# Kernel optimization log

Hardware: AMD Instinct MI355X
Metric: run time of the kernel (lower is better)

Reference implementation:

```python
import jax, jax.numpy as jnp
import numpy as np

EPS = 1e-5

def conv1x1(x, w):
    # x: [N,C,H,W], w: [O,C] (1x1 conv, no bias)
    return jnp.einsum('nchw,oc->nohw', x, w)

def bn_relu(x, gamma, beta, mean, var):
    # inference-mode BatchNorm2d + ReLU; params broadcast over H,W
    scale = gamma * jax.lax.rsqrt(var + EPS)
    y = (x - mean[:, None, None]) * scale[:, None, None] + beta[:, None, None]
    return jax.nn.relu(y)

def setup_inputs() -> dict:
    key = jax.random.key(0)
    ks = jax.random.split(key, 8)
    N, C, D, H, W = 4, 256, 9, 64, 64
    IC = C // 2
    return {
        'feature': jax.random.normal(ks[0], (N, C, D, H, W), dtype=jnp.float32),
        'w_theta': jax.random.normal(ks[1], (IC, C), dtype=jnp.float32) * 0.05,
        'bn_theta_gamma': jnp.ones((IC,), jnp.float32),
        'bn_theta_beta': jnp.zeros((IC,), jnp.float32),
        'bn_theta_mean': jax.random.normal(ks[2], (IC,), dtype=jnp.float32) * 0.1,
        'bn_theta_var': jax.random.uniform(ks[3], (IC,), dtype=jnp.float32, minval=0.5, maxval=1.5),
        'w_phi': jax.random.normal(ks[4], (IC, C), dtype=jnp.float32) * 0.05,
        'bn_phi_gamma': jnp.ones((IC,), jnp.float32),
        'bn_phi_beta': jnp.zeros((IC,), jnp.float32),
        'bn_phi_mean': jax.random.normal(ks[5], (IC,), dtype=jnp.float32) * 0.1,
        'bn_phi_var': jax.random.uniform(ks[6], (IC,), dtype=jnp.float32, minval=0.5, maxval=1.5),
        'w_g': jax.random.normal(ks[7], (IC, C), dtype=jnp.float32) * 0.05,
        'w_w': jax.random.normal(jax.random.fold_in(key, 99), (C, IC), dtype=jnp.float32) * 0.05,
    }

def reference(feature, w_theta, bn_theta_gamma, bn_theta_beta, bn_theta_mean, bn_theta_var,
              w_phi, bn_phi_gamma, bn_phi_beta, bn_phi_mean, bn_phi_var, w_g, w_w):
    N, C, D, H, W = feature.shape
    IC = w_theta.shape[0]
    center_x = feature[:, :, D // 2 + 1]               # [N,C,H,W]
    x = jnp.max(feature, axis=2)                       # max_pool3d (D,1,1) -> [N,C,H,W]

    theta = bn_relu(conv1x1(center_x, w_theta), bn_theta_gamma, bn_theta_beta, bn_theta_mean, bn_theta_var)
    phi = bn_relu(conv1x1(x, w_phi), bn_phi_gamma, bn_phi_beta, bn_phi_mean, bn_phi_var)
    g = conv1x1(x, w_g)

    HW = H * W
    theta_f = theta.reshape(N, IC, HW)                 # [N,IC,HW]
    phi_f = phi.reshape(N, IC, HW)
    g_f = g.reshape(N, IC, HW)

    f = jnp.einsum('ncq,nck->nqk', theta_f, phi_f)     # [N,HW,HW] unscaled scores
    weight = jax.nn.softmax(f, axis=-1)
    weighted = jnp.einsum('nqk,nck->ncq', weight, g_f) # [N,IC,HW]
    weighted = weighted.reshape(N, IC, H, W)

    out = conv1x1(weighted, w_w) + center_x            # residual
    return out
```

## Files before the change

### kernel.cpp

```cpp
#include <hip/hip_runtime.h>
#include <math.h>

#define HW   4096
#define CIN  256
#define ICH  128
#define NB   4
#define KSPL 6
#define KVB  32

typedef __attribute__((ext_vector_type(4))) float f32x4;
typedef __attribute__((ext_vector_type(8))) short bf16x8;
typedef __attribute__((ext_vector_type(4))) short bf16x4;
typedef __attribute__((ext_vector_type(4))) unsigned u32x4;

__device__ inline short f2bf(float f) {
    unsigned int u = __float_as_uint(f);
    u += 0x7fffU + ((u >> 16) & 1U);
    return (short)(u >> 16);
}

__device__ inline float bf2f(short s) {
    return __uint_as_float(((unsigned int)(unsigned short)s) << 16);
}

__device__ inline float exp2a(float x) {
    float r;
    asm("v_exp_f32 %0, %1" : "=v"(r) : "v"(x));
    return r;
}
__device__ inline float log2a(float x) {
    float r;
    asm("v_log_f32 %0, %1" : "=v"(r) : "v"(x));
    return r;
}
__device__ inline unsigned cvtpk(float a, float b) {
    unsigned r;
    asm("v_cvt_pk_bf16_f32 %0, %1, %2" : "=v"(r) : "v"(a), "v"(b));
    return r;
}

__device__ inline f32x4 mfma16(bf16x8 a, bf16x8 b, f32x4 c) {
    return __builtin_amdgcn_mfma_f32_16x16x32_bf16(a, b, c, 0, 0, 0);
}

__device__ inline bf16x8 ldf(const short* p) { return *(const bf16x8*)p; }

__global__ void k_prep_w(const float* __restrict__ wth, const float* __restrict__ wph,
                         const float* __restrict__ wg,  const float* __restrict__ ww,
                         const float* __restrict__ gth, const float* __restrict__ bth,
                         const float* __restrict__ mth, const float* __restrict__ vth,
                         const float* __restrict__ gph, const float* __restrict__ bph,
                         const float* __restrict__ mph, const float* __restrict__ vph,
                         short* __restrict__ wthb, short* __restrict__ wphb,
                         short* __restrict__ wgb,  short* __restrict__ wwb,
                         float* __restrict__ bnp) {
    const float LOG2E = 1.44269504f;
    int i = blockIdx.x * 256 + threadIdx.x;
    wthb[i] = f2bf(wth[i]);
    wphb[i] = f2bf(wph[i]);
    wgb[i]  = f2bf(wg[i]);
    wwb[i]  = f2bf(ww[i]);
    if (blockIdx.x == 0 && threadIdx.x < ICH) {
        int o = threadIdx.x;
        float s1 = gth[o] * rsqrtf(vth[o] + 1e-5f);
        bnp[o]        = s1 * LOG2E;
        bnp[ICH + o]  = (bth[o] - mth[o] * s1) * LOG2E;
        float s2 = gph[o] * rsqrtf(vph[o] + 1e-5f);
        bnp[2*ICH + o] = s2;
        bnp[3*ICH + o] = bph[o] - mph[o] * s2;
    }
}

__global__ __launch_bounds__(256) void k_prep_x(const float* __restrict__ feat,
                                                short* __restrict__ Xbf,
                                                short* __restrict__ CXbf) {
    const int q0 = blockIdx.x * 64;
    const int c0 = blockIdx.y * 32;
    const int n  = blockIdx.z;
    __shared__ float xs[32][68];
    __shared__ float cxs[32][68];
    const int tid = threadIdx.x;
    const int qv  = (tid & 15) * 4;
    const int ci  = tid >> 4;

    #pragma unroll
    for (int h = 0; h < 2; ++h) {
        const int cc = h * 16 + ci;
        const float* fp = feat + ((size_t)(n * CIN + c0 + cc)) * 9 * HW + q0 + qv;
        float4 mx = *(const float4*)fp;
        float4 cx = make_float4(0.f, 0.f, 0.f, 0.f);
        #pragma unroll
        for (int d = 1; d < 9; ++d) {
            float4 v = *(const float4*)(fp + (size_t)d * HW);
            if (d == 5) cx = v;
            mx.x = fmaxf(mx.x, v.x); mx.y = fmaxf(mx.y, v.y);
            mx.z = fmaxf(mx.z, v.z); mx.w = fmaxf(mx.w, v.w);
        }
        *(float4*)&xs[cc][qv]  = mx;
        *(float4*)&cxs[cc][qv] = cx;
    }
    __syncthreads();
    #pragma unroll
    for (int it = 0; it < 2; ++it) {
        const int q  = it * 32 + (tid >> 3);
        const int cq = (tid & 7) * 4;
        ushort4 ox, oc;
        ox.x = (unsigned short)f2bf(xs[cq][q]);
        ox.y = (unsigned short)f2bf(xs[cq + 1][q]);
        ox.z = (unsigned short)f2bf(xs[cq + 2][q]);
        ox.w = (unsigned short)f2bf(xs[cq + 3][q]);
        oc.x = (unsigned short)f2bf(cxs[cq][q]);
        oc.y = (unsigned short)f2bf(cxs[cq + 1][q]);
        oc.z = (unsigned short)f2bf(cxs[cq + 2][q]);
        oc.w = (unsigned short)f2bf(cxs[cq + 3][q]);
        const size_t ob = ((size_t)n * HW + q0 + q) * CIN + c0 + cq;
        *(ushort4*)&Xbf[ob]  = ox;
        *(ushort4*)&CXbf[ob] = oc;
    }
}

__global__ __launch_bounds__(256) void k_conv3(const short* __restrict__ Xbf,
                                               const short* __restrict__ CXbf,
                                               const short* __restrict__ wthb,
                                               const short* __restrict__ wphb,
                                               const short* __restrict__ wgb,
                                               const float* __restrict__ bnp,
                                               short* __restrict__ theta,
                                               short* __restrict__ phi,
                                               short* __restrict__ Vt) {
    const int n    = blockIdx.y;
    const int op   = blockIdx.z;
    const int wave = threadIdx.x >> 6;
    const int lane = threadIdx.x & 63;
    const int lr = lane & 15, lg = lane >> 4;
    const int q0 = blockIdx.x * 64 + wave * 16;
    const short* Xn  = Xbf  + (size_t)n * HW * CIN;
    const short* CXn = CXbf + (size_t)n * HW * CIN;

    f32x4 acc[8];
    #pragma unroll
    for (int i = 0; i < 8; ++i) { acc[i][0]=0.f; acc[i][1]=0.f; acc[i][2]=0.f; acc[i][3]=0.f; }

    if (op == 0) {
        short* thn = theta + (size_t)n * HW * ICH;
        #pragma unroll
        for (int cf = 0; cf < 8; ++cf) {
            bf16x8 a = ldf(CXn + (q0 + lr) * CIN + cf * 32 + lg * 8);
            #pragma unroll
            for (int of = 0; of < 8; ++of) {
                bf16x8 b = ldf(wthb + (of * 16 + lr) * CIN + cf * 32 + lg * 8);
                acc[of] = mfma16(a, b, acc[of]);
            }
        }
        #pragma unroll
        for (int of = 0; of < 8; ++of) {
            int o = of * 16 + lr;
            float sA = bnp[o], sB = bnp[ICH + o];
            #pragma unroll
            for (int r = 0; r < 4; ++r) {
                int q = q0 + lg * 4 + r;
                thn[q * ICH + o] = f2bf(fmaxf(acc[of][r] * sA + sB, 0.f));
            }
        }
    } else if (op == 1) {
        short* phn = phi + (size_t)n * HW * ICH;
        #pragma unroll
        for (int cf = 0; cf < 8; ++cf) {
            bf16x8 a = ldf(Xn + (q0 + lr) * CIN + cf * 32 + lg * 8);
            #pragma unroll
            for (int of = 0; of < 8; ++of) {
                bf16x8 b = ldf(wphb + (of * 16 + lr) * CIN + cf * 32 + lg * 8);
                acc[of] = mfma16(a, b, acc[of]);
            }
        }
        #pragma unroll
        for (int of = 0; of < 8; ++of) {
            int o = of * 16 + lr;
            float sA = bnp[2*ICH + o], sB = bnp[3*ICH + o];
            #pragma unroll
            for (int r = 0; r < 4; ++r) {
                int q = q0 + lg * 4 + r;
                phn[q * ICH + o] = f2bf(fmaxf(acc[of][r] * sA + sB, 0.f));
            }
        }
    } else {
        short* vtn = Vt + (size_t)n * ICH * HW;
        #pragma unroll
        for (int cf = 0; cf < 8; ++cf) {
            bf16x8 bx = ldf(Xn + (q0 + lr) * CIN + cf * 32 + lg * 8);
            #pragma unroll
            for (int mf = 0; mf < 8; ++mf) {
                bf16x8 a = ldf(wgb + (mf * 16 + lr) * CIN + cf * 32 + lg * 8);
                acc[mf] = mfma16(a, bx, acc[mf]);
            }
        }
        #pragma unroll
        for (int mf = 0; mf < 8; ++mf) {
            #pragma unroll
            for (int r = 0; r < 4; ++r) {
                int o = mf * 16 + lg * 4 + r;
                vtn[(size_t)o * HW + q0 + lr] = f2bf(acc[mf][r]);
            }
        }
    }
}

__global__ __launch_bounds__(256, 3) void k_attn(const short* __restrict__ theta,
                                                 const short* __restrict__ phi,
                                                 const short* __restrict__ Vt,
                                                 short* __restrict__ Op,
                                                 float* __restrict__ Ls) {
    __shared__ char  K_lds[2][8192];
    __shared__ short V_lds[2][128 * 40];

    const int bid  = blockIdx.x;
    const int j    = bid & 7;
    const int n    = j >> 1;
    const int rest = ((bid >> 3) << 1) | (j & 1);
    const int qb   = rest / KSPL;
    const int ks   = rest % KSPL;
    const int tbase = ks * 21 + (ks < 2 ? ks : 2);
    const int tcnt  = 21 + (ks < 2 ? 1 : 0);
    const int tid  = threadIdx.x;
    const int wave = tid >> 6;
    const int lane = tid & 63;
    const int lr = lane & 15, lg = lane >> 4;
    const int q0 = qb * 128 + wave * 32;

    const short* Qn = theta + (size_t)n * HW * ICH;
    const short* Kn = phi   + (size_t)n * HW * ICH;
    const short* Vn = Vt    + (size_t)n * ICH * HW;

    bf16x8 aq[2][4];
    #pragma unroll
    for (int m2 = 0; m2 < 2; ++m2)
        #pragma unroll
        for (int cf = 0; cf < 4; ++cf)
            aq[m2][cf] = ldf(Qn + (q0 + m2 * 16 + lr) * ICH + cf * 32 + lg * 8);

    f32x4 O[2][8];
    #pragma unroll
    for (int m2 = 0; m2 < 2; ++m2)
        #pragma unroll
        for (int i = 0; i < 8; ++i) { O[m2][i][0]=0.f; O[m2][i][1]=0.f; O[m2][i][2]=0.f; O[m2][i][3]=0.f; }
    float mx[2] = { -INFINITY, -INFINITY };
    float l[2]  = { 0.f, 0.f };

    bf16x8 kr0, kr1, vr0, vr1;
    auto loadK = [&](int tabs) {
        const char* kc = (const char*)(Kn + (size_t)tabs * KVB * ICH);
        kr0 = *(const bf16x8*)(kc + tid * 16);
        kr1 = *(const bf16x8*)(kc + 4096 + tid * 16);
    };
    auto writeK = [&](int pp) {
        const int o0 = tid * 16;
        const int o1 = 4096 + tid * 16;
        *(bf16x8*)&K_lds[pp][o0 ^ (((o0 >> 8) & 7) << 4)] = kr0;
        *(bf16x8*)&K_lds[pp][o1 ^ (((o1 >> 8) & 7) << 4)] = kr1;
    };
    auto loadV = [&](int tabs) {
        vr0 = ldf(Vn + (size_t)(tid >> 2) * HW + tabs * KVB + (tid & 3) * 8);
        vr1 = ldf(Vn + (size_t)((tid + 256) >> 2) * HW + tabs * KVB + (tid & 3) * 8);
    };
    auto writeV = [&](int pp) {
        *(bf16x8*)&V_lds[pp][(tid >> 2) * 40 + (tid & 3) * 8] = vr0;
        *(bf16x8*)&V_lds[pp][((tid + 256) >> 2) * 40 + (tid & 3) * 8] = vr1;
    };

    loadK(tbase);
    loadV(tbase);
    writeK(0);
    writeV(0);
    __syncthreads();

    for (int t = 0; t < tcnt; ++t) {
        const int p = t & 1;
        const bool pre = (t + 1 < tcnt);
        if (pre) { loadK(tbase + t + 1); loadV(tbase + t + 1); }

        f32x4 s[2][2];
        #pragma unroll
        for (int tt = 0; tt < 2; ++tt)
            #pragma unroll
            for (int m2 = 0; m2 < 2; ++m2) { s[tt][m2][0]=0.f; s[tt][m2][1]=0.f; s[tt][m2][2]=0.f; s[tt][m2][3]=0.f; }
        __builtin_amdgcn_s_setprio(1);
        #pragma unroll
        for (int tt = 0; tt < 2; ++tt) {
            const int row = tt * 16 + lr;
            const int rsw = (row & 7) << 4;
            #pragma unroll
            for (int cf = 0; cf < 4; ++cf) {
                bf16x8 kf = *(const bf16x8*)(&K_lds[p][row * 256 + ((cf * 64 + lg * 16) ^ rsw)]);
                s[tt][0] = mfma16(kf, aq[0][cf], s[tt][0]);
                s[tt][1] = mfma16(kf, aq[1][cf], s[tt][1]);
            }
        }
        __builtin_amdgcn_s_setprio(0);

        float lm[2];
        #pragma unroll
        for (int m2 = 0; m2 < 2; ++m2) {
            float a0 = fmaxf(fmaxf(s[0][m2][0], s[0][m2][1]), fmaxf(s[0][m2][2], s[0][m2][3]));
            float a1 = fmaxf(fmaxf(s[1][m2][0], s[1][m2][1]), fmaxf(s[1][m2][2], s[1][m2][3]));
            lm[m2] = fmaxf(a0, a1);
        }
        int need = (lm[0] > mx[0] + 11.f) || (lm[1] > mx[1] + 11.f);
        if (__any(need)) {
            #pragma unroll
            for (int m2 = 0; m2 < 2; ++m2) {
                float v = lm[m2];
                v = fmaxf(v, __shfl_xor(v, 16));
                v = fmaxf(v, __shfl_xor(v, 32));
                float mn = fmaxf(mx[m2], v);
                float a  = exp2a(mx[m2] - mn);
                mx[m2] = mn;
                l[m2] *= a;
                #pragma unroll
                for (int cc = 0; cc < 8; ++cc) {
                    O[m2][cc][0] *= a; O[m2][cc][1] *= a;
                    O[m2][cc][2] *= a; O[m2][cc][3] *= a;
                }
            }
        }
        bf16x8 pb[2];
        #pragma unroll
        for (int m2 = 0; m2 < 2; ++m2) {
            float e[8];
            #pragma unroll
            for (int r = 0; r < 4; ++r) {
                e[r]     = exp2a(s[0][m2][r] - mx[m2]);
                e[4 + r] = exp2a(s[1][m2][r] - mx[m2]);
            }
            l[m2] += ((e[0] + e[1]) + (e[2] + e[3])) + ((e[4] + e[5]) + (e[6] + e[7]));
            union { u32x4 u; bf16x8 b; } cv;
            cv.u[0] = cvtpk(e[0], e[1]);
            cv.u[1] = cvtpk(e[2], e[3]);
            cv.u[2] = cvtpk(e[4], e[5]);
            cv.u[3] = cvtpk(e[6], e[7]);
            pb[m2] = cv.b;
        }

        __builtin_amdgcn_s_setprio(1);
        #pragma unroll
        for (int cc = 0; cc < 8; ++cc) {
            const short* vb = &V_lds[p][(cc * 16 + lr) * 40 + lg * 4];
            bf16x4 va0 = *(const bf16x4*)vb;
            bf16x4 va1 = *(const bf16x4*)(vb + 16);
            bf16x8 vf = __builtin_shufflevector(va0, va1, 0, 1, 2, 3, 4, 5, 6, 7);
            O[0][cc] = mfma16(vf, pb[0], O[0][cc]);
            O[1][cc] = mfma16(vf, pb[1], O[1][cc]);
        }
        __builtin_amdgcn_s_setprio(0);

        if (pre) { writeK(p ^ 1); writeV(p ^ 1); }
        __syncthreads();
    }

    const size_t obase = (size_t)(ks * NB + n) * HW;
    #pragma unroll
    for (int m2 = 0; m2 < 2; ++m2) {
        float v = l[m2];
        v += __shfl_xor(v, 16);
        v += __shfl_xor(v, 32);
        l[m2] = v;
        const float inv = 1.f / v;
        const int q = q0 + m2 * 16 + lr;
        #pragma unroll
        for (int cc = 0; cc < 8; ++cc) {
            uint2 ov;
            ov.x = cvtpk(O[m2][cc][0] * inv, O[m2][cc][1] * inv);
            ov.y = cvtpk(O[m2][cc][2] * inv, O[m2][cc][3] * inv);
            *(uint2*)&Op[(obase + q) * ICH + cc * 16 + lg * 4] = ov;
        }
        if (lg == 0)
            Ls[obase + q] = mx[m2] + log2a(l[m2]);
    }
}

__global__ __launch_bounds__(256) void k_out(const short* __restrict__ Op,
                                             const float* __restrict__ Ls,
                                             const short* __restrict__ wwb,
                                             const float* __restrict__ feat,
                                             float* __restrict__ out) {
    __shared__ char bo_lds[32 * 256];
    const int n   = blockIdx.y;
    const int q0  = blockIdx.x * 32;
    const int tid = threadIdx.x;

    {
        const int q  = tid >> 3;
        const int c0 = (tid & 7) * 16;
        const int qg = q0 + q;
        float ls[KSPL], M = -INFINITY;
        #pragma unroll
        for (int i = 0; i < KSPL; ++i) {
            ls[i] = Ls[((size_t)(i * NB + n)) * HW + qg];
            M = fmaxf(M, ls[i]);
        }
        float wq[KSPL], ws = 0.f;
        #pragma unroll
        for (int i = 0; i < KSPL; ++i) { wq[i] = exp2a(ls[i] - M); ws += wq[i]; }
        const float inv = 1.f / ws;
        float fo[16];
        #pragma unroll
        for (int e = 0; e < 16; ++e) fo[e] = 0.f;
        #pragma unroll
        for (int i = 0; i < KSPL; ++i) {
            const short* p = Op + ((size_t)(i * NB + n) * HW + qg) * ICH + c0;
            bf16x8 v0 = ldf(p);
            bf16x8 v1 = ldf(p + 8);
            #pragma unroll
            for (int e = 0; e < 8; ++e) {
                fo[e]     += wq[i] * bf2f(v0[e]);
                fo[8 + e] += wq[i] * bf2f(v1[e]);
            }
        }
        const int rsw = (q & 7) << 4;
        u32x4 w0, w1;
        #pragma unroll
        for (int e = 0; e < 4; ++e) {
            w0[e] = cvtpk(fo[2*e] * inv,     fo[2*e+1] * inv);
            w1[e] = cvtpk(fo[8+2*e] * inv,   fo[8+2*e+1] * inv);
        }
        *(u32x4*)&bo_lds[q * 256 + ((c0 * 2) ^ rsw)]        = w0;
        *(u32x4*)&bo_lds[q * 256 + (((c0 + 8) * 2) ^ rsw)]  = w1;
    }
    __syncthreads();

    const int wave = tid >> 6;
    const int lane = tid & 63;
    const int lr = lane & 15, lg = lane >> 4;
    const int o0 = wave * 64;

    f32x4 acc[4][2];
    #pragma unroll
    for (int i = 0; i < 4; ++i)
        #pragma unroll
        for (int jn = 0; jn < 2; ++jn) { acc[i][jn][0]=0.f; acc[i][jn][1]=0.f; acc[i][jn][2]=0.f; acc[i][jn][3]=0.f; }

    #pragma unroll
    for (int cf = 0; cf < 4; ++cf) {
        bf16x8 bO[2];
        #pragma unroll
        for (int nf = 0; nf < 2; ++nf) {
            const int row = nf * 16 + lr;
            const int byt = (cf * 64 + lg * 16) ^ ((row & 7) << 4);
            bO[nf] = *(const bf16x8*)&bo_lds[row * 256 + byt];
        }
        #pragma unroll
        for (int mf = 0; mf < 4; ++mf) {
            bf16x8 a = ldf(wwb + (o0 + mf * 16 + lr) * ICH + cf * 32 + lg * 8);
            #pragma unroll
            for (int nf = 0; nf < 2; ++nf)
                acc[mf][nf] = mfma16(a, bO[nf], acc[mf][nf]);
        }
    }
    #pragma unroll
    for (int mf = 0; mf < 4; ++mf) {
        #pragma unroll
        for (int nf = 0; nf < 2; ++nf) {
            #pragma unroll
            for (int r = 0; r < 4; ++r) {
                int o = o0 + mf * 16 + lg * 4 + r;
                int q = q0 + nf * 16 + lr;
                long long cxi = (((long long)(n * CIN + o)) * 9 + 5) * HW + q;
                out[((long long)(n * CIN + o)) * HW + q] = acc[mf][nf][r] + feat[cxi];
            }
        }
    }
}

extern "C" void kernel_launch(void* const* d_in, const int* in_sizes, int n_in,
                              void* d_out, int out_size, void* d_ws, size_t ws_size,
                              hipStream_t stream) {
    const float* feat = (const float*)d_in[0];
    const float* wth  = (const float*)d_in[1];
    const float* gth  = (const float*)d_in[2];
    const float* bth  = (const float*)d_in[3];
    const float* mth  = (const float*)d_in[4];
    const float* vth  = (const float*)d_in[5];
    const float* wph  = (const float*)d_in[6];
    const float* gph  = (const float*)d_in[7];
    const float* bph  = (const float*)d_in[8];
    const float* mph  = (const float*)d_in[9];
    const float* vph  = (const float*)d_in[10];
    const float* wg   = (const float*)d_in[11];
    const float* ww   = (const float*)d_in[12];
    float* out = (float*)d_out;

    size_t off = 0;
    auto carve = [&](size_t bytes) {
        void* p = (char*)d_ws + off;
        off += (bytes + 255) & ~(size_t)255;
        return p;
    };
    short* Xbf   = (short*)carve((size_t)NB * HW * CIN * 2);
    short* CXbf  = (short*)carve((size_t)NB * HW * CIN * 2);
    short* theta = (short*)carve((size_t)NB * HW * ICH * 2);
    short* phi   = (short*)carve((size_t)NB * HW * ICH * 2);
    short* Vt    = (short*)carve((size_t)NB * ICH * HW * 2);
    short* Op    = (short*)carve((size_t)KSPL * NB * HW * ICH * 2);
    float* Ls    = (float*)carve((size_t)KSPL * NB * HW * 4);
    short* wthb  = (short*)carve((size_t)ICH * CIN * 2);
    short* wphb  = (short*)carve((size_t)ICH * CIN * 2);
    short* wgb   = (short*)carve((size_t)ICH * CIN * 2);
    short* wwb   = (short*)carve((size_t)CIN * ICH * 2);
    float* bnp   = (float*)carve((size_t)4 * ICH * 4);

    k_prep_w<<<128, 256, 0, stream>>>(wth, wph, wg, ww, gth, bth, mth, vth,
                                      gph, bph, mph, vph, wthb, wphb, wgb, wwb, bnp);
    k_prep_x<<<dim3(64, 8, NB), 256, 0, stream>>>(feat, Xbf, CXbf);
    k_conv3<<<dim3(64, NB, 3), 256, 0, stream>>>(Xbf, CXbf, wthb, wphb, wgb, bnp,
                                                 theta, phi, Vt);
    k_attn<<<768, 256, 0, stream>>>(theta, phi, Vt, Op, Ls);
    k_out<<<dim3(128, NB), 256, 0, stream>>>(Op, Ls, wwb, feat, out);
}
```

Before: 119.8 us.

## Software-pipeline QK of next tile with PV of current; fold weight prep into prep_x

The attention loop is restructured so the QK^T MFMAs for the next K tile are issued right after the barrier, before the PV MFMAs of the current tile. This lets softmax math overlap with matrix work, and V now uses a triple-buffered LDS ring to avoid hazards. Separately, the weight bf16 conversion and BN parameter folding are merged into the k_prep_x kernel to remove one launch. The cost is extra LDS for the third V buffer, which may lower occupancy, and higher register pressure from keeping s and pb live across iterations.

```diff
diff --git a/kernel.cpp b/kernel.cpp
--- a/kernel.cpp
+++ b/kernel.cpp
@@ -45,41 +45,55 @@
 
 __device__ inline bf16x8 ldf(const short* p) { return *(const bf16x8*)p; }
 
-__global__ void k_prep_w(const float* __restrict__ wth, const float* __restrict__ wph,
-                         const float* __restrict__ wg,  const float* __restrict__ ww,
-                         const float* __restrict__ gth, const float* __restrict__ bth,
-                         const float* __restrict__ mth, const float* __restrict__ vth,
-                         const float* __restrict__ gph, const float* __restrict__ bph,
-                         const float* __restrict__ mph, const float* __restrict__ vph,
-                         short* __restrict__ wthb, short* __restrict__ wphb,
-                         short* __restrict__ wgb,  short* __restrict__ wwb,
-                         float* __restrict__ bnp) {
-    const float LOG2E = 1.44269504f;
-    int i = blockIdx.x * 256 + threadIdx.x;
-    wthb[i] = f2bf(wth[i]);
-    wphb[i] = f2bf(wph[i]);
-    wgb[i]  = f2bf(wg[i]);
-    wwb[i]  = f2bf(ww[i]);
-    if (blockIdx.x == 0 && threadIdx.x < ICH) {
-        int o = threadIdx.x;
-        float s1 = gth[o] * rsqrtf(vth[o] + 1e-5f);
-        bnp[o]        = s1 * LOG2E;
-        bnp[ICH + o]  = (bth[o] - mth[o] * s1) * LOG2E;
-        float s2 = gph[o] * rsqrtf(vph[o] + 1e-5f);
-        bnp[2*ICH + o] = s2;
-        bnp[3*ICH + o] = bph[o] - mph[o] * s2;
-    }
-}
-
 __global__ __launch_bounds__(256) void k_prep_x(const float* __restrict__ feat,
                                                 short* __restrict__ Xbf,
-                                                short* __restrict__ CXbf) {
+                                                short* __restrict__ CXbf,
+                                                const float* __restrict__ wth,
+                                                const float* __restrict__ wph,
+                                                const float* __restrict__ wg,
+                                                const float* __restrict__ ww,
+                                                const float* __restrict__ gth,
+                                                const float* __restrict__ bth,
+                                                const float* __restrict__ mth,
+                                                const float* __restrict__ vth,
+                                                const float* __restrict__ gph,
+                                                const float* __restrict__ bph,
+                                                const float* __restrict__ mph,
+                                                const float* __restrict__ vph,
+                                                short* __restrict__ wthb,
+                                                short* __restrict__ wphb,
+                                                short* __restrict__ wgb,
+                                                short* __restrict__ wwb,
+                                                float* __restrict__ bnp) {
+    const float LOG2E = 1.44269504f;
     const int q0 = blockIdx.x * 64;
     const int c0 = blockIdx.y * 32;
     const int n  = blockIdx.z;
     __shared__ float xs[32][68];
     __shared__ float cxs[32][68];
     const int tid = threadIdx.x;
+
+    if (blockIdx.y == 0) {
+        const int wid = blockIdx.x + 64 * n;
+        const int i = wid * 128 + (tid & 127);
+        if (tid < 128) {
+            wthb[i] = f2bf(wth[i]);
+            wphb[i] = f2bf(wph[i]);
+        } else {
+            wgb[i] = f2bf(wg[i]);
+            wwb[i] = f2bf(ww[i]);
+        }
+        if (wid == 0 && tid < ICH) {
+            int o = tid;
+            float s1 = gth[o] * rsqrtf(vth[o] + 1e-5f);
+            bnp[o]        = s1 * LOG2E;
+            bnp[ICH + o]  = (bth[o] - mth[o] * s1) * LOG2E;
+            float s2 = gph[o] * rsqrtf(vph[o] + 1e-5f);
+            bnp[2*ICH + o] = s2;
+            bnp[3*ICH + o] = bph[o] - mph[o] * s2;
+        }
+    }
+
     const int qv  = (tid & 15) * 4;
     const int ci  = tid >> 4;
 
@@ -211,7 +225,7 @@
                                                  short* __restrict__ Op,
                                                  float* __restrict__ Ls) {
     __shared__ char  K_lds[2][8192];
-    __shared__ short V_lds[2][128 * 40];
+    __shared__ short V_lds[3][128 * 40];
 
     const int bid  = blockIdx.x;
     const int j    = bid & 7;
@@ -222,8 +236,8 @@
     const int tbase = ks * 21 + (ks < 2 ? ks : 2);
     const int tcnt  = 21 + (ks < 2 ? 1 : 0);
     const int tid  = threadIdx.x;
+    const int lane = tid & 63;
     const int wave = tid >> 6;
-    const int lane = tid & 63;
     const int lr = lane & 15, lg = lane >> 4;
     const int q0 = qb * 128 + wave * 32;
 
@@ -246,7 +260,10 @@
     float mx[2] = { -INFINITY, -INFINITY };
     float l[2]  = { 0.f, 0.f };
 
+    f32x4  s[2][2];
+    bf16x8 pb[2];
     bf16x8 kr0, kr1, vr0, vr1;
+
     auto loadK = [&](int tabs) {
         const char* kc = (const char*)(Kn + (size_t)tabs * KVB * ICH);
         kr0 = *(const bf16x8*)(kc + tid * 16);
@@ -266,36 +283,50 @@
         *(bf16x8*)&V_lds[pp][(tid >> 2) * 40 + (tid & 3) * 8] = vr0;
         *(bf16x8*)&V_lds[pp][((tid + 256) >> 2) * 40 + (tid & 3) * 8] = vr1;
     };
+    auto qk = [&](int pp) {
+        #pragma unroll
+        for (int tt = 0; tt < 2; ++tt)
+            #pragma unroll
+            for (int m2 = 0; m2 < 2; ++m2) { s[tt][m2][0]=0.f; s[tt][m2][1]=0.f; s[tt][m2][2]=0.f; s[tt][m2][3]=0.f; }
+        __builtin_amdgcn_s_setprio(1);
+        #pragma unroll
+        for (int tt = 0; tt < 2; ++tt) {
+            const int row = tt * 16 + lr;
+            const int rsw = (row & 7) << 4;
+            #pragma unroll
+            for (int cf = 0; cf < 4; ++cf) {
+                bf16x8 kf = *(const bf16x8*)(&K_lds[pp][row * 256 + ((cf * 64 + lg * 16) ^ rsw)]);
+                s[tt][0] = mfma16(kf, aq[0][cf], s[tt][0]);
+                s[tt][1] = mfma16(kf, aq[1][cf], s[tt][1]);
+            }
+        }
+        __builtin_amdgcn_s_setprio(0);
+    };
+    auto pv = [&](int pp) {
+        __builtin_amdgcn_s_setprio(1);
+        #pragma unroll
+        for (int cc = 0; cc < 8; ++cc) {
+            const short* vb = &V_lds[pp][(cc * 16 + lr) * 40 + lg * 4];
+            bf16x4 va0 = *(const bf16x4*)vb;
+            bf16x4 va1 = *(const bf16x4*)(vb + 16);
+            bf16x8 vf = __builtin_shufflevector(va0, va1, 0, 1, 2, 3, 4, 5, 6, 7);
+            O[0][cc] = mfma16(vf, pb[0], O[0][cc]);
+            O[1][cc] = mfma16(vf, pb[1], O[1][cc]);
+        }
+        __builtin_amdgcn_s_setprio(0);
+    };
 
     loadK(tbase);
     loadV(tbase);
     writeK(0);
     writeV(0);
     __syncthreads();
-
+    qk(0);
+
+    int vw = 1;
     for (int t = 0; t < tcnt; ++t) {
-        const int p = t & 1;
         const bool pre = (t + 1 < tcnt);
         if (pre) { loadK(tbase + t + 1); loadV(tbase + t + 1); }
-
-        f32x4 s[2][2];
-        #pragma unroll
-        for (int tt = 0; tt < 2; ++tt)
-            #pragma unroll
-            for (int m2 = 0; m2 < 2; ++m2) { s[tt][m2][0]=0.f; s[tt][m2][1]=0.f; s[tt][m2][2]=0.f; s[tt][m2][3]=0.f; }
-        __builtin_amdgcn_s_setprio(1);
-        #pragma unroll
-        for (int tt = 0; tt < 2; ++tt) {
-            const int row = tt * 16 + lr;
-            const int rsw = (row & 7) << 4;
-            #pragma unroll
-            for (int cf = 0; cf < 4; ++cf) {
-                bf16x8 kf = *(const bf16x8*)(&K_lds[p][row * 256 + ((cf * 64 + lg * 16) ^ rsw)]);
-                s[tt][0] = mfma16(kf, aq[0][cf], s[tt][0]);
-                s[tt][1] = mfma16(kf, aq[1][cf], s[tt][1]);
-            }
-        }
-        __builtin_amdgcn_s_setprio(0);
 
         float lm[2];
         #pragma unroll
@@ -322,7 +353,6 @@
                 }
             }
         }
-        bf16x8 pb[2];
         #pragma unroll
         for (int m2 = 0; m2 < 2; ++m2) {
             float e[8];
@@ -340,20 +370,12 @@
             pb[m2] = cv.b;
         }
 
-        __builtin_amdgcn_s_setprio(1);
-        #pragma unroll
-        for (int cc = 0; cc < 8; ++cc) {
-            const short* vb = &V_lds[p][(cc * 16 + lr) * 40 + lg * 4];
-            bf16x4 va0 = *(const bf16x4*)vb;
-            bf16x4 va1 = *(const bf16x4*)(vb + 16);
-            bf16x8 vf = __builtin_shufflevector(va0, va1, 0, 1, 2, 3, 4, 5, 6, 7);
-            O[0][cc] = mfma16(vf, pb[0], O[0][cc]);
-            O[1][cc] = mfma16(vf, pb[1], O[1][cc]);
-        }
-        __builtin_amdgcn_s_setprio(0);
-
-        if (pre) { writeK(p ^ 1); writeV(p ^ 1); }
+        if (pre) { writeK((t + 1) & 1); writeV(vw); }
         __syncthreads();
+
+        if (pre) qk((t + 1) & 1);
+        pv(vw == 0 ? 2 : vw - 1);
+        vw = (vw == 2) ? 0 : vw + 1;
     }
 
     const size_t obase = (size_t)(ks * NB + n) * HW;
@@ -507,9 +529,11 @@
     short* wwb   = (short*)carve((size_t)CIN * ICH * 2);
     float* bnp   = (float*)carve((size_t)4 * ICH * 4);
 
-    k_prep_w<<<128, 256, 0, stream>>>(wth, wph, wg, ww, gth, bth, mth, vth,
-                                      gph, bph, mph, vph, wthb, wphb, wgb, wwb, bnp);
-    k_prep_x<<<dim3(64, 8, NB), 256, 0, stream>>>(feat, Xbf, CXbf);
+    k_prep_x<<<dim3(64, 8, NB), 256, 0, stream>>>(feat, Xbf, CXbf,
+                                                  wth, wph, wg, ww,
+                                                  gth, bth, mth, vth,
+                                                  gph, bph, mph, vph,
+                                                  wthb, wphb, wgb, wwb, bnp);
     k_conv3<<<dim3(64, NB, 3), 256, 0, stream>>>(Xbf, CXbf, wthb, wphb, wgb, bnp,
                                                  theta, phi, Vt);
     k_attn<<<768, 256, 0, stream>>>(theta, phi, Vt, Op, Ls);
```

Result: faster. 114.6 us (-4.4%).
